# Performance work log

Hardware: AMD Instinct MI355X
Metric: run time of the kernel (lower is better)

## Reference

```python
import jax, jax.numpy as jnp
import numpy as np

B1, B2, N, D = 1, 128, 256, 256
H, C = 8, 32
OUT = 256


def setup_inputs() -> dict:
    key = jax.random.key(0)
    ks = jax.random.split(key, 8)
    in_data = jax.random.normal(ks[0], (B1, B2, N, D), dtype=jnp.float32)
    # binary mask, mostly unmasked
    mask = (jax.random.uniform(ks[1], (B1, B2, N)) > 0.1).astype(jnp.float32)
    nonbatched_bias = jax.random.normal(ks[2], (B1, H, N, N), dtype=jnp.float32)
    scale = 1.0 / np.sqrt(D)
    w_qkv = jax.random.normal(ks[3], (3 * H * C, D), dtype=jnp.float32) * scale  # torch Linear [out,in]
    w_gate = jax.random.normal(ks[4], (H * C, D), dtype=jnp.float32) * scale
    gating_bias = jnp.ones((H * C,), dtype=jnp.float32)
    w_o = jax.random.normal(ks[5], (OUT, H * C), dtype=jnp.float32) * scale
    b_o = jnp.zeros((OUT,), dtype=jnp.float32)
    return {
        "in_data": in_data,
        "mask": mask,
        "nonbatched_bias": nonbatched_bias,
        "w_qkv": w_qkv,
        "w_gate": w_gate,
        "gating_bias": gating_bias,
        "w_o": w_o,
        "b_o": b_o,
    }


def reference(in_data, mask, nonbatched_bias, w_qkv, w_gate, gating_bias, w_o, b_o):
    scaling = C ** (-0.5)
    # fused QKV projection (no bias): [b1,b2,n, 3*h*c]
    qkv = jnp.einsum("xynd,ed->xyne", in_data, w_qkv)
    q, k, v = jnp.split(qkv, 3, axis=-1)

    def heads(t):  # [b1,b2,n,h*c] -> [b1,b2,h,n,c]
        return t.reshape(B1, B2, N, H, C).transpose(0, 1, 3, 2, 4)

    q, k, v = heads(q) * scaling, heads(k), heads(v)
    logits = jnp.einsum("xyhqc,xyhkc->xyhqk", q, k)
    mask_bias = (1e9 * (mask - 1.0))[:, :, None, None, :]  # [b1,b2,1,1,n]
    logits = logits + mask_bias + nonbatched_bias[:, None]  # [b1,b2,h,q,k]
    weights = jax.nn.softmax(logits, axis=-1)
    wa = jnp.einsum("xyhqk,xyhkc->xyhqc", weights, v)
    wa = wa.transpose(0, 1, 3, 2, 4).reshape(B1, B2, N, H * C)
    # sigmoid gating: sigmoid(gate_linear(x) + gating_bias) * weighted_avg
    gate = jax.nn.sigmoid(jnp.einsum("xynd,ed->xyne", in_data, w_gate) + gating_bias)
    wa = gate * wa
    out = jnp.einsum("xyne,oe->xyno", wa, w_o) + b_o
    return out
```

## Files before the change

kernel.cpp:

```cpp
#include <hip/hip_runtime.h>
#include <stdint.h>

#define B2 128
#define NSEQ 256
#define DIM 256
#define NH 8
#define CH 32

typedef __attribute__((ext_vector_type(8))) __bf16 bf16x8;
typedef __attribute__((ext_vector_type(8))) unsigned short u16x8;
typedef __attribute__((ext_vector_type(4))) unsigned short u16x4;
typedef __attribute__((ext_vector_type(4))) unsigned int u32x4;
typedef __attribute__((ext_vector_type(4))) float f32x4;

__device__ __forceinline__ unsigned short f2bf(float f) {
  unsigned int u = __builtin_bit_cast(unsigned int, f);
  u += 0x7FFFu + ((u >> 16) & 1u);
  return (unsigned short)(u >> 16);
}
__device__ __forceinline__ float bf2f(unsigned short h) {
  unsigned int u = ((unsigned int)h) << 16;
  return __builtin_bit_cast(float, u);
}
__device__ __forceinline__ bf16x8 as_bf(u16x8 v) { return __builtin_bit_cast(bf16x8, v); }

__device__ __forceinline__ void gload16(void* lds, const void* g) {
  __builtin_amdgcn_global_load_lds(
      (__attribute__((address_space(1))) void*)(g),
      (__attribute__((address_space(3))) void*)(lds), 16, 0, 0);
}

__global__ void k_convert(const float* __restrict__ x, const float* __restrict__ wqkv,
                          const float* __restrict__ wgate, const float* __restrict__ wo,
                          const float* __restrict__ nb,
                          unsigned short* __restrict__ xb, unsigned short* __restrict__ wallb,
                          unsigned short* __restrict__ wob, unsigned short* __restrict__ nbb) {
  const int NX = 8388608, NWALL = 262144, NWO = 65536, NNB = 524288;
  int i = blockIdx.x * blockDim.x + threadIdx.x;
  int total4 = (NX + NWALL + NWO + NNB) >> 2;
  if (i >= total4) return;
  int e = i << 2;
  float4 v;
  unsigned short* dst;
  if (e < NX) {
    v = *reinterpret_cast<const float4*>(x + e);
    dst = xb + e;
  } else if (e < NX + NWALL) {
    int o = e - NX;
    v = (o < 196608) ? *reinterpret_cast<const float4*>(wqkv + o)
                     : *reinterpret_cast<const float4*>(wgate + (o - 196608));
    dst = wallb + o;
  } else if (e < NX + NWALL + NWO) {
    int o = e - NX - NWALL;
    v = *reinterpret_cast<const float4*>(wo + o);
    dst = wob + o;
  } else {
    int o = e - NX - NWALL - NWO;
    v = *reinterpret_cast<const float4*>(nb + o);
    dst = nbb + o;
  }
  u16x4 r;
  r[0] = f2bf(v.x); r[1] = f2bf(v.y); r[2] = f2bf(v.z); r[3] = f2bf(v.w);
  *reinterpret_cast<u16x4*>(dst) = r;
}

__launch_bounds__(512, 3)
__global__ void k_gemm0(const unsigned short* __restrict__ Ab, const unsigned short* __restrict__ Bw,
                        unsigned short* __restrict__ qs, unsigned short* __restrict__ ksb,
                        unsigned short* __restrict__ vsb, unsigned short* __restrict__ gateb,
                        const float* __restrict__ gbias) {
  __shared__ __attribute__((aligned(16))) char smem[49152];
  const int tid = threadIdx.x, lane = tid & 63, w = tid >> 6;
  const int wr = w >> 2, wc = w & 3;
  const int l15 = lane & 15, hi = lane >> 4;
  const int m0 = blockIdx.x * 128, n0 = blockIdx.y * 256;

  auto stageA = [&](int buf, int k0) {
    char* sbuf = buf ? smem + 8192 : smem;
    int i = tid;
    int rp = i >> 3, sp = i & 7;
    int sl = sp ^ (rp & 7);
    int row = 2 * rp + (sl >> 2), s3 = sl & 3;
    const unsigned short* g = Ab + (size_t)(m0 + row) * 256 + k0 + s3 * 8;
    gload16(sbuf + w * 1024, g);
  };
  auto stageB = [&](int buf, int k0) {
    char* sbuf = buf ? smem + 32768 : smem + 16384;
#pragma unroll
    for (int q2 = 0; q2 < 2; ++q2) {
      int i = q2 * 512 + tid;
      int rp = i >> 3, sp = i & 7;
      int sl = sp ^ (rp & 7);
      int row = 2 * rp + (sl >> 2), s3 = sl & 3;
      const unsigned short* g = Bw + (size_t)(n0 + row) * 256 + k0 + s3 * 8;
      gload16(sbuf + q2 * 8192 + w * 1024, g);
    }
  };

  f32x4 acc[4][4];
#pragma unroll
  for (int i = 0; i < 4; ++i) {
#pragma unroll
    for (int j = 0; j < 4; ++j) acc[i][j] = (f32x4){0.f, 0.f, 0.f, 0.f};
  }

  stageA(0, 0);
  stageB(0, 0);

#pragma unroll
  for (int kt = 0; kt < 8; ++kt) {
    const int cur = kt & 1;
    asm volatile("s_waitcnt vmcnt(0)" ::: "memory");
    __builtin_amdgcn_sched_barrier(0);
    __builtin_amdgcn_s_barrier();
    __builtin_amdgcn_sched_barrier(0);
    if (kt < 7) {
      stageA(cur ^ 1, (kt + 1) * 32);
      stageB(cur ^ 1, (kt + 1) * 32);
    }
    {
      const char* Acur = cur ? smem + 8192 : smem;
      const char* Bcur = cur ? smem + 32768 : smem + 16384;
      bf16x8 af[4], bfv[4];
#pragma unroll
      for (int fr = 0; fr < 4; ++fr) {
        int ra = wr * 64 + fr * 16 + l15;
        int rp = ra >> 1;
        int sl = ((ra & 1) << 2) | hi;
        int off = rp * 128 + (sl ^ (rp & 7)) * 16;
        af[fr] = *reinterpret_cast<const bf16x8*>(Acur + off);
      }
#pragma unroll
      for (int fc = 0; fc < 4; ++fc) {
        int rb = wc * 64 + fc * 16 + l15;
        int rp = rb >> 1;
        int sl = ((rb & 1) << 2) | hi;
        int off = rp * 128 + (sl ^ (rp & 7)) * 16;
        bfv[fc] = *reinterpret_cast<const bf16x8*>(Bcur + off);
      }
#pragma unroll
      for (int fr = 0; fr < 4; ++fr) {
#pragma unroll
        for (int fc = 0; fc < 4; ++fc)
          acc[fr][fc] = __builtin_amdgcn_mfma_f32_16x16x32_bf16(af[fr], bfv[fc], acc[fr][fc], 0, 0, 0);
      }
    }
  }

  const int which = blockIdx.y;
  unsigned short* ep = reinterpret_cast<unsigned short*>(smem);
  float gb4[4];
  if (which == 3) {
#pragma unroll
    for (int fc = 0; fc < 4; ++fc) gb4[fc] = gbias[wc * 64 + fc * 16 + l15];
  }
  unsigned short* dstbuf = (which == 0) ? qs : (which == 1) ? ksb : (which == 2) ? vsb : gateb;
#pragma unroll
  for (int half = 0; half < 2; ++half) {
    __syncthreads();
    if (wr == half) {
#pragma unroll
      for (int fr = 0; fr < 4; ++fr) {
#pragma unroll
        for (int fc = 0; fc < 4; ++fc) {
          int col = wc * 64 + fc * 16 + l15;
#pragma unroll
          for (int i = 0; i < 4; ++i) {
            float v = acc[fr][fc][i];
            if (which == 0) v *= 0.17677669529663687f;
            if (which == 3) v = 1.0f / (1.0f + __expf(-(v + gb4[fc])));
            ep[(fr * 16 + (hi << 2) + i) * 264 + col] = f2bf(v);
          }
        }
      }
    }
    __syncthreads();
    const int row = tid >> 3, hh = tid & 7;
    const int mrow2 = m0 + half * 64 + row;
    const int b = mrow2 >> 8, n = mrow2 & 255;
    unsigned short* dst = dstbuf + ((size_t)(b * 8 + hh) * 256 + n) * 32;
    const unsigned short* src = ep + row * 264 + hh * 32;
#pragma unroll
    for (int q4 = 0; q4 < 4; ++q4)
      *reinterpret_cast<u16x8*>(dst + q4 * 8) = *reinterpret_cast<const u16x8*>(src + q4 * 8);
  }
}

__launch_bounds__(256, 4)
__global__ void k_gemm1(const unsigned short* __restrict__ Ab, const unsigned short* __restrict__ Bw,
                        float* __restrict__ outp, const float* __restrict__ bo) {
  __shared__ __attribute__((aligned(16))) char As[2][8192];
  __shared__ __attribute__((aligned(16))) char Bs[2][8192];
  const int tid = threadIdx.x, lane = tid & 63, w = tid >> 6;
  const int wr = w >> 1, wc = w & 1;
  const int l15 = lane & 15, hi = lane >> 4;
  const int m0 = blockIdx.x * 128, n0 = blockIdx.y * 128;

  auto stage_pair = [&](char* sbuf, const unsigned short* gsrc, int row0, int k0) {
#pragma unroll
    for (int q2 = 0; q2 < 2; ++q2) {
      int i = q2 * 256 + tid;
      int rp = i >> 3, sp = i & 7;
      int sl = sp ^ (rp & 7);
      int row = 2 * rp + (sl >> 2), s3 = sl & 3;
      const unsigned short* g = gsrc + (size_t)(row0 + row) * 256 + k0 + s3 * 8;
      gload16(sbuf + q2 * 4096 + w * 1024, g);
    }
  };

  f32x4 acc[4][4];
#pragma unroll
  for (int i = 0; i < 4; ++i) {
#pragma unroll
    for (int j = 0; j < 4; ++j) acc[i][j] = (f32x4){0.f, 0.f, 0.f, 0.f};
  }

  stage_pair(As[0], Ab, m0, 0);
  stage_pair(Bs[0], Bw, n0, 0);

#pragma unroll
  for (int kt = 0; kt < 8; ++kt) {
    const int cur = kt & 1;
    asm volatile("s_waitcnt vmcnt(0)" ::: "memory");
    __builtin_amdgcn_sched_barrier(0);
    __builtin_amdgcn_s_barrier();
    __builtin_amdgcn_sched_barrier(0);
    if (kt < 7) {
      stage_pair(As[cur ^ 1], Ab, m0, (kt + 1) * 32);
      stage_pair(Bs[cur ^ 1], Bw, n0, (kt + 1) * 32);
    }
    {
      bf16x8 af[4], bfv[4];
#pragma unroll
      for (int fr = 0; fr < 4; ++fr) {
        int ra = wr * 64 + fr * 16 + l15;
        int rp = ra >> 1;
        int sl = ((ra & 1) << 2) | hi;
        int off = rp * 128 + (sl ^ (rp & 7)) * 16;
        af[fr] = *reinterpret_cast<const bf16x8*>(As[cur] + off);
      }
#pragma unroll
      for (int fc = 0; fc < 4; ++fc) {
        int rb = wc * 64 + fc * 16 + l15;
        int rp = rb >> 1;
        int sl = ((rb & 1) << 2) | hi;
        int off = rp * 128 + (sl ^ (rp & 7)) * 16;
        bfv[fc] = *reinterpret_cast<const bf16x8*>(Bs[cur] + off);
      }
#pragma unroll
      for (int fr = 0; fr < 4; ++fr) {
#pragma unroll
        for (int fc = 0; fc < 4; ++fc)
          acc[fr][fc] = __builtin_amdgcn_mfma_f32_16x16x32_bf16(af[fr], bfv[fc], acc[fr][fc], 0, 0, 0);
      }
    }
  }

#pragma unroll
  for (int fr = 0; fr < 4; ++fr) {
    int mrow = m0 + wr * 64 + fr * 16 + (hi << 2);
#pragma unroll
    for (int fc = 0; fc < 4; ++fc) {
      int e = n0 + wc * 64 + fc * 16 + l15;
      float bb = bo[e];
#pragma unroll
      for (int i = 0; i < 4; ++i)
        outp[(size_t)(mrow + i) * 256 + e] = acc[fr][fc][i] + bb;
    }
  }
}

__launch_bounds__(512, 2)
__global__ void k_attn(const unsigned short* __restrict__ qs, const unsigned short* __restrict__ ksb,
                       const unsigned short* __restrict__ vsb, const unsigned short* __restrict__ gateb,
                       const float* __restrict__ mask, const unsigned short* __restrict__ nbb,
                       unsigned short* __restrict__ wag) {
  __shared__ __attribute__((aligned(16))) unsigned short vt[32][264];
  __shared__ __attribute__((aligned(16))) unsigned short pch[8][16][72];
  __shared__ __attribute__((aligned(16))) unsigned short Kl[16][64][8];
  __shared__ __attribute__((aligned(16))) float mb[256];
  __shared__ float invl[8][16];
  const int tid = threadIdx.x, lane = tid & 63, w = tid >> 6;
  const int l15 = lane & 15, hi = lane >> 4;
  const int b = blockIdx.x, h = blockIdx.y;
  const size_t bh = (size_t)(b * 8 + h);
  const unsigned short* kbase = ksb + bh * 8192;
  const unsigned short* vbase = vsb + bh * 8192;
  const unsigned short* qbase = qs + bh * 8192;
  const unsigned short* nbh = nbb + (size_t)h * 65536;

  if (tid < 256) {
    mb[tid] = 1e9f * (mask[b * 256 + tid] - 1.0f);
    const unsigned short* vrow = vbase + tid * 32;
#pragma unroll
    for (int c0 = 0; c0 < 32; c0 += 8) {
      u16x8 vv = *reinterpret_cast<const u16x8*>(vrow + c0);
#pragma unroll
      for (int j = 0; j < 8; ++j) vt[c0 + j][tid] = vv[j];
    }
  } else {
    const int key = tid - 256;
    const unsigned short* krow = kbase + key * 32;
#pragma unroll
    for (int c8 = 0; c8 < 4; ++c8)
      *reinterpret_cast<u16x8*>(&Kl[key >> 4][c8 * 16 + (key & 15)][0]) =
          *reinterpret_cast<const u16x8*>(krow + c8 * 8);
  }
  __syncthreads();

  const f32x4 zero = {0.f, 0.f, 0.f, 0.f};
#pragma unroll 1
  for (int fr = 0; fr < 2; ++fr) {
    const int q0 = w * 32 + fr * 16;
    u16x8 qf = *reinterpret_cast<const u16x8*>(qbase + (q0 + l15) * 32 + hi * 8);

    const unsigned short* nbq = nbh + (size_t)(q0 + l15) * 256;
    u16x4 nbv[16];
#pragma unroll
    for (int kt = 0; kt < 16; ++kt)
      nbv[kt] = *reinterpret_cast<const u16x4*>(nbq + kt * 16 + hi * 4);

    f32x4 sacc[16];
    __builtin_amdgcn_s_setprio(1);
#pragma unroll
    for (int kt = 0; kt < 16; ++kt) {
      bf16x8 kf = *reinterpret_cast<const bf16x8*>(&Kl[kt][lane][0]);
      sacc[kt] = __builtin_amdgcn_mfma_f32_16x16x32_bf16(kf, as_bf(qf), zero, 0, 0, 0);
    }
    __builtin_amdgcn_s_setprio(0);

#pragma unroll
    for (int kt = 0; kt < 16; ++kt) {
      float4 mb4 = *reinterpret_cast<const float4*>(&mb[kt * 16 + hi * 4]);
      sacc[kt][0] += mb4.x + bf2f(nbv[kt][0]);
      sacc[kt][1] += mb4.y + bf2f(nbv[kt][1]);
      sacc[kt][2] += mb4.z + bf2f(nbv[kt][2]);
      sacc[kt][3] += mb4.w + bf2f(nbv[kt][3]);
    }
    float mx = -3.0e38f;
#pragma unroll
    for (int kt = 0; kt < 16; ++kt) {
#pragma unroll
      for (int i = 0; i < 4; ++i) mx = fmaxf(mx, sacc[kt][i]);
    }
    mx = fmaxf(mx, __shfl_xor(mx, 16));
    mx = fmaxf(mx, __shfl_xor(mx, 32));

    float sum = 0.f;
    f32x4 wacc[2];
    wacc[0] = zero; wacc[1] = zero;
#pragma unroll
    for (int c = 0; c < 4; ++c) {
#pragma unroll
      for (int ktl = 0; ktl < 4; ++ktl) {
        const int kt = c * 4 + ktl;
        u16x4 pv;
#pragma unroll
        for (int i = 0; i < 4; ++i) {
          float p = __expf(sacc[kt][i] - mx);
          sum += p;
          pv[i] = f2bf(p);
        }
        *reinterpret_cast<u16x4*>(&pch[w][l15][ktl * 16 + hi * 4]) = pv;
      }
      asm volatile("" ::: "memory");
      __builtin_amdgcn_s_setprio(1);
#pragma unroll
      for (int ks2 = 0; ks2 < 2; ++ks2) {
        bf16x8 pa = *reinterpret_cast<const bf16x8*>(&pch[w][l15][ks2 * 32 + hi * 8]);
#pragma unroll
        for (int ct = 0; ct < 2; ++ct) {
          bf16x8 vb = *reinterpret_cast<const bf16x8*>(&vt[ct * 16 + l15][c * 64 + ks2 * 32 + hi * 8]);
          wacc[ct] = __builtin_amdgcn_mfma_f32_16x16x32_bf16(pa, vb, wacc[ct], 0, 0, 0);
        }
      }
      __builtin_amdgcn_s_setprio(0);
    }
    sum += __shfl_xor(sum, 16);
    sum += __shfl_xor(sum, 32);
    const float inv = 1.0f / sum;
    if (hi == 0) invl[w][l15] = inv;

    asm volatile("" ::: "memory");
    float* et = reinterpret_cast<float*>(&pch[w][0][0]);
#pragma unroll
    for (int ct = 0; ct < 2; ++ct) {
#pragma unroll
      for (int i = 0; i < 4; ++i)
        et[(hi * 4 + i) * 36 + ct * 16 + l15] = wacc[ct][i];
    }
    asm volatile("" ::: "memory");
    const int eq = lane >> 2, eh = lane & 3;
    float4 v0 = *reinterpret_cast<const float4*>(&et[eq * 36 + eh * 8]);
    float4 v1 = *reinterpret_cast<const float4*>(&et[eq * 36 + eh * 8 + 4]);
    const float iv = invl[w][eq];
    const int qrow = q0 + eq;
    u16x8 g = *reinterpret_cast<const u16x8*>(gateb + bh * 8192 + qrow * 32 + eh * 8);
    u16x8 ov;
    ov[0] = f2bf(bf2f(g[0]) * v0.x * iv);
    ov[1] = f2bf(bf2f(g[1]) * v0.y * iv);
    ov[2] = f2bf(bf2f(g[2]) * v0.z * iv);
    ov[3] = f2bf(bf2f(g[3]) * v0.w * iv);
    ov[4] = f2bf(bf2f(g[4]) * v1.x * iv);
    ov[5] = f2bf(bf2f(g[5]) * v1.y * iv);
    ov[6] = f2bf(bf2f(g[6]) * v1.z * iv);
    ov[7] = f2bf(bf2f(g[7]) * v1.w * iv);
    *reinterpret_cast<u16x8*>(wag + ((size_t)(b * 256 + qrow)) * 256 + h * 32 + eh * 8) = ov;
    asm volatile("" ::: "memory");
  }
}

extern "C" void kernel_launch(void* const* d_in, const int* in_sizes, int n_in,
                              void* d_out, int out_size, void* d_ws, size_t ws_size,
                              hipStream_t stream) {
  const float* x     = (const float*)d_in[0];
  const float* mask  = (const float*)d_in[1];
  const float* nb    = (const float*)d_in[2];
  const float* wqkv  = (const float*)d_in[3];
  const float* wgate = (const float*)d_in[4];
  const float* gbias = (const float*)d_in[5];
  const float* wo    = (const float*)d_in[6];
  const float* bo    = (const float*)d_in[7];
  float* outp = (float*)d_out;

  char* ws = (char*)d_ws;
  unsigned short* xb    = (unsigned short*)(ws);
  unsigned short* wallb = (unsigned short*)(ws + 16777216);
  unsigned short* wob   = (unsigned short*)(ws + 17301504);
  unsigned short* qs    = (unsigned short*)(ws + 17432576);
  unsigned short* ksb   = (unsigned short*)(ws + 34209792);
  unsigned short* vsb   = (unsigned short*)(ws + 50987008);
  unsigned short* gateb = (unsigned short*)(ws + 67764224);
  unsigned short* nbb   = (unsigned short*)(ws + 84541440);
  unsigned short* wag   = xb;

  k_convert<<<dim3(9024), dim3(256), 0, stream>>>(x, wqkv, wgate, wo, nb, xb, wallb, wob, nbb);
  k_gemm0<<<dim3(256, 4), dim3(512), 0, stream>>>(xb, wallb, qs, ksb, vsb, gateb, gbias);
  k_attn<<<dim3(128, 8), dim3(512), 0, stream>>>(qs, ksb, vsb, gateb, mask, nbb, wag);
  k_gemm1<<<dim3(256, 2), dim3(256), 0, stream>>>(wag, wob, outp, bo);
}
```

Baseline: 116.1 us.

## Fuse fp32-to-bf16 conversion of activations into QKV/gate GEMM loads

The separate conversion pass over the large fp32 input is dropped. The first GEMM now streams fp32 activation tiles straight into LDS and converts them to bf16 with packed convert instructions while building MFMA fragments. This removes a full read-convert-write round trip of the input. In exchange, A-tile LDS traffic and footprint double (64KB shared memory), occupancy drops from 3 to 2 blocks per CU, and the same A tile is converted redundantly by the four column-wave groups.

```diff
diff --git a/kernel.cpp b/kernel.cpp
--- a/kernel.cpp
+++ b/kernel.cpp
@@ -23,6 +23,11 @@
   return __builtin_bit_cast(float, u);
 }
 __device__ __forceinline__ bf16x8 as_bf(u16x8 v) { return __builtin_bit_cast(bf16x8, v); }
+__device__ __forceinline__ unsigned int cvtpk(float lo, float hi) {
+  unsigned int r;
+  asm("v_cvt_pk_bf16_f32 %0, %1, %2" : "=v"(r) : "v"(lo), "v"(hi));
+  return r;
+}
 
 __device__ __forceinline__ void gload16(void* lds, const void* g) {
   __builtin_amdgcn_global_load_lds(
@@ -30,32 +35,27 @@
       (__attribute__((address_space(3))) void*)(lds), 16, 0, 0);
 }
 
-__global__ void k_convert(const float* __restrict__ x, const float* __restrict__ wqkv,
-                          const float* __restrict__ wgate, const float* __restrict__ wo,
-                          const float* __restrict__ nb,
-                          unsigned short* __restrict__ xb, unsigned short* __restrict__ wallb,
-                          unsigned short* __restrict__ wob, unsigned short* __restrict__ nbb) {
-  const int NX = 8388608, NWALL = 262144, NWO = 65536, NNB = 524288;
+__global__ void k_convert(const float* __restrict__ wqkv, const float* __restrict__ wgate,
+                          const float* __restrict__ wo, const float* __restrict__ nb,
+                          unsigned short* __restrict__ wallb, unsigned short* __restrict__ wob,
+                          unsigned short* __restrict__ nbb) {
+  const int NWALL = 262144, NWO = 65536, NNB = 524288;
   int i = blockIdx.x * blockDim.x + threadIdx.x;
-  int total4 = (NX + NWALL + NWO + NNB) >> 2;
+  int total4 = (NWALL + NWO + NNB) >> 2;
   if (i >= total4) return;
   int e = i << 2;
   float4 v;
   unsigned short* dst;
-  if (e < NX) {
-    v = *reinterpret_cast<const float4*>(x + e);
-    dst = xb + e;
-  } else if (e < NX + NWALL) {
-    int o = e - NX;
-    v = (o < 196608) ? *reinterpret_cast<const float4*>(wqkv + o)
-                     : *reinterpret_cast<const float4*>(wgate + (o - 196608));
-    dst = wallb + o;
-  } else if (e < NX + NWALL + NWO) {
-    int o = e - NX - NWALL;
+  if (e < NWALL) {
+    v = (e < 196608) ? *reinterpret_cast<const float4*>(wqkv + e)
+                     : *reinterpret_cast<const float4*>(wgate + (e - 196608));
+    dst = wallb + e;
+  } else if (e < NWALL + NWO) {
+    int o = e - NWALL;
     v = *reinterpret_cast<const float4*>(wo + o);
     dst = wob + o;
   } else {
-    int o = e - NX - NWALL - NWO;
+    int o = e - NWALL - NWO;
     v = *reinterpret_cast<const float4*>(nb + o);
     dst = nbb + o;
   }
@@ -64,28 +64,30 @@
   *reinterpret_cast<u16x4*>(dst) = r;
 }
 
-__launch_bounds__(512, 3)
-__global__ void k_gemm0(const unsigned short* __restrict__ Ab, const unsigned short* __restrict__ Bw,
+__launch_bounds__(512, 2)
+__global__ void k_gemm0(const float* __restrict__ Af, const unsigned short* __restrict__ Bw,
                         unsigned short* __restrict__ qs, unsigned short* __restrict__ ksb,
                         unsigned short* __restrict__ vsb, unsigned short* __restrict__ gateb,
                         const float* __restrict__ gbias) {
-  __shared__ __attribute__((aligned(16))) char smem[49152];
+  __shared__ __attribute__((aligned(16))) char smem[65536];
   const int tid = threadIdx.x, lane = tid & 63, w = tid >> 6;
   const int wr = w >> 2, wc = w & 3;
   const int l15 = lane & 15, hi = lane >> 4;
   const int m0 = blockIdx.x * 128, n0 = blockIdx.y * 256;
 
   auto stageA = [&](int buf, int k0) {
-    char* sbuf = buf ? smem + 8192 : smem;
-    int i = tid;
-    int rp = i >> 3, sp = i & 7;
-    int sl = sp ^ (rp & 7);
-    int row = 2 * rp + (sl >> 2), s3 = sl & 3;
-    const unsigned short* g = Ab + (size_t)(m0 + row) * 256 + k0 + s3 * 8;
-    gload16(sbuf + w * 1024, g);
+    char* sbuf = buf ? smem + 16384 : smem;
+#pragma unroll
+    for (int q2 = 0; q2 < 2; ++q2) {
+      int i = q2 * 512 + tid;
+      int r = i >> 3, sp = i & 7;
+      int sl = sp ^ (r & 7);
+      const float* g = Af + (size_t)(m0 + r) * 256 + k0 + sl * 4;
+      gload16(sbuf + q2 * 8192 + w * 1024, g);
+    }
   };
   auto stageB = [&](int buf, int k0) {
-    char* sbuf = buf ? smem + 32768 : smem + 16384;
+    char* sbuf = buf ? smem + 49152 : smem + 32768;
 #pragma unroll
     for (int q2 = 0; q2 < 2; ++q2) {
       int i = q2 * 512 + tid;
@@ -119,16 +121,22 @@
       stageB(cur ^ 1, (kt + 1) * 32);
     }
     {
-      const char* Acur = cur ? smem + 8192 : smem;
-      const char* Bcur = cur ? smem + 32768 : smem + 16384;
+      const char* Acur = cur ? smem + 16384 : smem;
+      const char* Bcur = cur ? smem + 49152 : smem + 32768;
       bf16x8 af[4], bfv[4];
 #pragma unroll
       for (int fr = 0; fr < 4; ++fr) {
         int ra = wr * 64 + fr * 16 + l15;
-        int rp = ra >> 1;
-        int sl = ((ra & 1) << 2) | hi;
-        int off = rp * 128 + (sl ^ (rp & 7)) * 16;
-        af[fr] = *reinterpret_cast<const bf16x8*>(Acur + off);
+        const char* base = Acur + ra * 128;
+        int sw = (ra & 7) << 4;
+        f32x4 a0 = *reinterpret_cast<const f32x4*>(base + ((hi * 32) ^ sw));
+        f32x4 a1 = *reinterpret_cast<const f32x4*>(base + ((hi * 32 + 16) ^ sw));
+        u32x4 afu;
+        afu[0] = cvtpk(a0[0], a0[1]);
+        afu[1] = cvtpk(a0[2], a0[3]);
+        afu[2] = cvtpk(a1[0], a1[1]);
+        afu[3] = cvtpk(a1[2], a1[3]);
+        af[fr] = __builtin_bit_cast(bf16x8, afu);
       }
 #pragma unroll
       for (int fc = 0; fc < 4; ++fc) {
@@ -424,7 +432,7 @@
   float* outp = (float*)d_out;
 
   char* ws = (char*)d_ws;
-  unsigned short* xb    = (unsigned short*)(ws);
+  unsigned short* wag   = (unsigned short*)(ws);
   unsigned short* wallb = (unsigned short*)(ws + 16777216);
   unsigned short* wob   = (unsigned short*)(ws + 17301504);
   unsigned short* qs    = (unsigned short*)(ws + 17432576);
@@ -432,10 +440,9 @@
   unsigned short* vsb   = (unsigned short*)(ws + 50987008);
   unsigned short* gateb = (unsigned short*)(ws + 67764224);
   unsigned short* nbb   = (unsigned short*)(ws + 84541440);
-  unsigned short* wag   = xb;
-
-  k_convert<<<dim3(9024), dim3(256), 0, stream>>>(x, wqkv, wgate, wo, nb, xb, wallb, wob, nbb);
-  k_gemm0<<<dim3(256, 4), dim3(512), 0, stream>>>(xb, wallb, qs, ksb, vsb, gateb, gbias);
+
+  k_convert<<<dim3(833), dim3(256), 0, stream>>>(wqkv, wgate, wo, nb, wallb, wob, nbb);
+  k_gemm0<<<dim3(256, 4), dim3(512), 0, stream>>>(x, wallb, qs, ksb, vsb, gateb, gbias);
   k_attn<<<dim3(128, 8), dim3(512), 0, stream>>>(qs, ksb, vsb, gateb, mask, nbb, wag);
   k_gemm1<<<dim3(256, 2), dim3(256), 0, stream>>>(wag, wob, outp, bo);
 }
```

Result: slower. 126.1 us (+8.6%).
